# Performance work log

Hardware: AMD Instinct MI355X
Metric: run time of the kernel (lower is better)

Reference implementation:

```python
import jax, jax.numpy as jnp
import numpy as np

K = 512  # number of clusters
D = 128  # feature dim
N = 8192 # number of points


def setup_inputs() -> dict:
    key = jax.random.key(0)
    k1, k2 = jax.random.split(key)
    locF = jax.random.normal(k1, (N, 1, D), dtype=jnp.float32)
    Ck = jax.random.normal(k2, (1, K, D), dtype=jnp.float32)
    return {"locF": locF, "Ck": Ck}


def reference(locF, Ck):
    # locF: [N, 1, D], Ck: [1, K, D]
    x = locF[:, 0, :]          # [N, D]
    c = Ck[0]                  # [K, D]
    # (GEMM expansion avoids the [N, K, D] broadcast; argmin is unchanged)
    d2 = ((x * x).sum(-1, keepdims=True)
          - 2.0 * (x @ c.T)
          + (c * c).sum(-1)[None, :]) / D   # [N, K]
    index = jnp.argmin(d2, axis=1)           # [N]
    # per-cluster scatter-sum and counts (fused, single pass)
    Ck1 = jax.ops.segment_sum(x, index, num_segments=K)[None]  # [1, K, D]
    nItems = jax.ops.segment_sum(jnp.ones((x.shape[0],), dtype=jnp.int32),
                                 index, num_segments=K).reshape(1, -1)  # [1, K]
    return (Ck1, nItems)
```

## Files before the change

### kernel.cpp

```cpp
#include <hip/hip_runtime.h>
#include <hip/hip_bf16.h>

#define KC 512
#define DD 128
#define NP 8192


__global__ __launch_bounds__(256) void kprep(const float* __restrict__ Ck,
                                             float* __restrict__ CkT,
                                             float* __restrict__ sumc2,
                                             float* __restrict__ out) {
    const int b = blockIdx.x;
    const int t = threadIdx.x;
    if (b < 32) {
        #pragma unroll
        for (int i = 0; i < 8; ++i) {
            const int idx = b * 2048 + i * 256 + t;
            const int d = idx >> 9;
            const int k = idx & 511;
            CkT[idx] = Ck[k * DD + d];
        }
    } else if (b == 32) {
        #pragma unroll
        for (int c = 0; c < 2; ++c) {
            const int k = t + c * 256;
            const float4* row = (const float4*)(Ck + k * DD);
            float s = 0.f;
            #pragma unroll
            for (int i = 0; i < 32; ++i) {
                const float4 v = row[i];
                s += v.x * v.x + v.y * v.y + v.z * v.z + v.w * v.w;
            }
            sumc2[k] = s;
        }
    } else {
        const int base = (b - 33) * 2048 + t;
        #pragma unroll
        for (int i = 0; i < 8; ++i) {
            const int idx = base + i * 256;
            if (idx < KC * DD + KC) out[idx] = 0.f;
        }
    }
}

__global__ __launch_bounds__(256, 1) void kmain(const float* __restrict__ X,
                                                const float* __restrict__ CkT,
                                                const float* __restrict__ sumc2,
                                                float* __restrict__ out) {
    __shared__ __align__(16) float xs[32 * DD];
    __shared__ __align__(16) float cst[16 * KC];
    __shared__ int win[32];

    const int tid  = threadIdx.x;
    const int lane = tid & 63;
    const int wv   = tid >> 6;
    const int p0   = blockIdx.x * 32;

    {
        const float4* Xv = (const float4*)(X + p0 * DD);
        float4* xv = (float4*)xs;
        #pragma unroll
        for (int i = 0; i < 4; ++i) xv[tid + 256 * i] = Xv[tid + 256 * i];
    }

    float acc[8][8];
    #pragma unroll
    for (int i = 0; i < 8; ++i)
        #pragma unroll
        for (int j = 0; j < 8; ++j) acc[i][j] = 0.f;

    for (int s = 0; s < 8; ++s) {
        __syncthreads();
        {
            const float4* Cv = (const float4*)(CkT + s * 16 * KC);
            float4* cv = (float4*)cst;
            #pragma unroll
            for (int i = 0; i < 8; ++i) cv[tid + 256 * i] = Cv[tid + 256 * i];
        }
        __syncthreads();

        #pragma unroll
        for (int kk4 = 0; kk4 < 4; ++kk4) {
            float4 xf[8];
            #pragma unroll
            for (int i = 0; i < 8; ++i)
                xf[i] = *(const float4*)&xs[(8 * wv + i) * DD + s * 16 + kk4 * 4];
            #pragma unroll
            for (int kk = 0; kk < 4; ++kk) {
                const float4 c0 = *(const float4*)&cst[(kk4 * 4 + kk) * KC + 4 * lane];
                const float4 c1 = *(const float4*)&cst[(kk4 * 4 + kk) * KC + 256 + 4 * lane];
                #pragma unroll
                for (int i = 0; i < 8; ++i) {
                    const float xv = (&xf[i].x)[kk];
                    acc[i][0] = fmaf(xv, c0.x, acc[i][0]);
                    acc[i][1] = fmaf(xv, c0.y, acc[i][1]);
                    acc[i][2] = fmaf(xv, c0.z, acc[i][2]);
                    acc[i][3] = fmaf(xv, c0.w, acc[i][3]);
                    acc[i][4] = fmaf(xv, c1.x, acc[i][4]);
                    acc[i][5] = fmaf(xv, c1.y, acc[i][5]);
                    acc[i][6] = fmaf(xv, c1.z, acc[i][6]);
                    acc[i][7] = fmaf(xv, c1.w, acc[i][7]);
                }
            }
        }
    }

    float bestv[8];
    int   besti[8];
    #pragma unroll
    for (int i = 0; i < 8; ++i) { bestv[i] = 3.4e38f; besti[i] = 0; }
    #pragma unroll
    for (int j = 0; j < 8; ++j) {
        const int cent = (j < 4) ? (4 * lane + j) : (256 + 4 * lane + (j - 4));
        const float s2 = sumc2[cent];
        #pragma unroll
        for (int i = 0; i < 8; ++i) {
            const float v = fmaf(-2.f, acc[i][j], s2);
            if (v < bestv[i]) { bestv[i] = v; besti[i] = cent; }
        }
    }
    #pragma unroll
    for (int off = 1; off < 64; off <<= 1) {
        #pragma unroll
        for (int i = 0; i < 8; ++i) {
            const float ov = __shfl_xor(bestv[i], off);
            const int   oi = __shfl_xor(besti[i], off);
            if (ov < bestv[i] || (ov == bestv[i] && oi < besti[i])) {
                bestv[i] = ov; besti[i] = oi;
            }
        }
    }
    if (lane == 0) {
        #pragma unroll
        for (int i = 0; i < 8; ++i) win[8 * wv + i] = besti[i];
    }
    __syncthreads();

    #pragma unroll
    for (int i = 0; i < 16; ++i) {
        const int flat = tid + 256 * i;
        const int p = flat >> 7;
        const int d = flat & 127;
        atomicAdd(&out[win[p] * DD + d], xs[flat]);
    }
    if (tid < 32) atomicAdd(&out[KC * DD + win[tid]], 1.0f);
}

extern "C" void kernel_launch(void* const* d_in, const int* in_sizes, int n_in,
                              void* d_out, int out_size, void* d_ws, size_t ws_size,
                              hipStream_t stream) {
    const float* locF = (const float*)d_in[0];
    const float* Ck   = (const float*)d_in[1];
    float* out   = (float*)d_out;
    float* sumc2 = (float*)d_ws;
    float* CkT   = (float*)((char*)d_ws + 4096);

    hipLaunchKernelGGL(kprep, dim3(66), dim3(256), 0, stream, Ck, CkT, sumc2, out);
    hipLaunchKernelGGL(kmain, dim3(256), dim3(256), 0, stream, locF, CkT, sumc2, out);
}
```

Baseline: 50.15 us.

## Split-K across wave halves with double-buffered direct-to-LDS centroid loads

Each block now handles 16 points instead of 32, so the grid grows to 512 blocks and occupancy rises to two blocks per CU. Within a block the two pairs of waves each take half of the feature dimension, and their partial dot products are summed through LDS before the argmin. Centroid tiles are streamed with global_load_lds into double-buffered shared memory, overlapping the next load with the current FMAs. This costs an extra LDS reduction and barrier, and each block now reads the full centroid table for fewer points.

```diff
diff --git a/kernel.cpp b/kernel.cpp
--- a/kernel.cpp
+++ b/kernel.cpp
@@ -5,6 +5,13 @@
 #define DD 128
 #define NP 8192
 
+
+__device__ __forceinline__ void gload_lds16(const float* g, float* l) {
+    __builtin_amdgcn_global_load_lds(
+        (const __attribute__((address_space(1))) void*)(uintptr_t)g,
+        (__attribute__((address_space(3))) void*)(uintptr_t)l,
+        16, 0, 0);
+}
 
 __global__ __launch_bounds__(256) void kprep(const float* __restrict__ Ck,
                                              float* __restrict__ CkT,
@@ -43,25 +50,38 @@
     }
 }
 
-__global__ __launch_bounds__(256, 1) void kmain(const float* __restrict__ X,
+__global__ __launch_bounds__(256, 2) void kmain(const float* __restrict__ X,
                                                 const float* __restrict__ CkT,
                                                 const float* __restrict__ sumc2,
                                                 float* __restrict__ out) {
-    __shared__ __align__(16) float xs[32 * DD];
-    __shared__ __align__(16) float cst[16 * KC];
-    __shared__ int win[32];
+    __shared__ __align__(16) float xs[16 * DD];
+    __shared__ __align__(16) float cst[2][2][8 * KC];
+    __shared__ int win[16];
 
     const int tid  = threadIdx.x;
     const int lane = tid & 63;
     const int wv   = tid >> 6;
-    const int p0   = blockIdx.x * 32;
-
-    {
-        const float4* Xv = (const float4*)(X + p0 * DD);
-        float4* xv = (float4*)xs;
-        #pragma unroll
-        for (int i = 0; i < 4; ++i) xv[tid + 256 * i] = Xv[tid + 256 * i];
-    }
+    const int h    = wv >> 1;
+    const int wl   = wv & 1;
+    const int p0   = blockIdx.x * 16;
+
+    const float* Xg = X + p0 * DD;
+    #pragma unroll
+    for (int j = 0; j < 2; ++j) {
+        const int unit = (wv * 2 + j) * 64;
+        gload_lds16(Xg + (unit + lane) * 4, &xs[unit * 4]);
+    }
+
+    auto STAGE = [&](int t, int b) {
+        const float* src = CkT + (h * 64 + t * 8) * KC;
+        float* dst = &cst[b][h][0];
+        #pragma unroll
+        for (int j = 0; j < 8; ++j) {
+            const int chunk = (wl * 8 + j) * 256;
+            gload_lds16(src + chunk + lane * 4, dst + chunk);
+        }
+    };
+    STAGE(0, 0);
 
     float acc[8][8];
     #pragma unroll
@@ -69,26 +89,29 @@
         #pragma unroll
         for (int j = 0; j < 8; ++j) acc[i][j] = 0.f;
 
-    for (int s = 0; s < 8; ++s) {
-        __syncthreads();
-        {
-            const float4* Cv = (const float4*)(CkT + s * 16 * KC);
-            float4* cv = (float4*)cst;
-            #pragma unroll
-            for (int i = 0; i < 8; ++i) cv[tid + 256 * i] = Cv[tid + 256 * i];
-        }
-        __syncthreads();
-
-        #pragma unroll
-        for (int kk4 = 0; kk4 < 4; ++kk4) {
+    for (int t = 0; t < 8; ++t) {
+        const int b = t & 1;
+        if (t < 7) {
+            STAGE(t + 1, b ^ 1);
+            asm volatile("s_waitcnt vmcnt(8)" ::: "memory");
+        } else {
+            asm volatile("s_waitcnt vmcnt(0)" ::: "memory");
+        }
+        __builtin_amdgcn_s_barrier();
+        __builtin_amdgcn_sched_barrier(0);
+
+        const float* cb = &cst[b][h][0];
+        const int dbase = h * 64 + t * 8;
+        #pragma unroll
+        for (int kk4 = 0; kk4 < 2; ++kk4) {
             float4 xf[8];
             #pragma unroll
             for (int i = 0; i < 8; ++i)
-                xf[i] = *(const float4*)&xs[(8 * wv + i) * DD + s * 16 + kk4 * 4];
+                xf[i] = *(const float4*)&xs[(8 * wl + i) * DD + dbase + kk4 * 4];
             #pragma unroll
             for (int kk = 0; kk < 4; ++kk) {
-                const float4 c0 = *(const float4*)&cst[(kk4 * 4 + kk) * KC + 4 * lane];
-                const float4 c1 = *(const float4*)&cst[(kk4 * 4 + kk) * KC + 256 + 4 * lane];
+                const float4 c0 = *(const float4*)&cb[(kk4 * 4 + kk) * KC + 4 * lane];
+                const float4 c1 = *(const float4*)&cb[(kk4 * 4 + kk) * KC + 256 + 4 * lane];
                 #pragma unroll
                 for (int i = 0; i < 8; ++i) {
                     const float xv = (&xf[i].x)[kk];
@@ -103,47 +126,69 @@
                 }
             }
         }
-    }
-
-    float bestv[8];
-    int   besti[8];
+        __builtin_amdgcn_sched_barrier(0);
+        __builtin_amdgcn_s_barrier();
+        __builtin_amdgcn_sched_barrier(0);
+    }
+
+    float4* ex = (float4*)&cst[0][0][0];
+    const int tl = tid & 127;
+    if (h == 1) {
+        #pragma unroll
+        for (int i = 0; i < 8; ++i) {
+            ex[(2 * i) * 128 + tl]     = make_float4(acc[i][0], acc[i][1], acc[i][2], acc[i][3]);
+            ex[(2 * i + 1) * 128 + tl] = make_float4(acc[i][4], acc[i][5], acc[i][6], acc[i][7]);
+        }
+    }
+    __syncthreads();
+    if (h == 0) {
+        #pragma unroll
+        for (int i = 0; i < 8; ++i) {
+            const float4 a0 = ex[(2 * i) * 128 + tl];
+            const float4 a1 = ex[(2 * i + 1) * 128 + tl];
+            acc[i][0] += a0.x; acc[i][1] += a0.y; acc[i][2] += a0.z; acc[i][3] += a0.w;
+            acc[i][4] += a1.x; acc[i][5] += a1.y; acc[i][6] += a1.z; acc[i][7] += a1.w;
+        }
+        float bestv[8];
+        int   besti[8];
+        #pragma unroll
+        for (int i = 0; i < 8; ++i) { bestv[i] = 3.4e38f; besti[i] = 0; }
+        #pragma unroll
+        for (int j = 0; j < 8; ++j) {
+            const int cent = (j < 4) ? (4 * lane + j) : (256 + 4 * lane + (j - 4));
+            const float s2 = sumc2[cent];
+            #pragma unroll
+            for (int i = 0; i < 8; ++i) {
+                const float v = fmaf(-2.f, acc[i][j], s2);
+                if (v < bestv[i]) { bestv[i] = v; besti[i] = cent; }
+            }
+        }
+        #pragma unroll
+        for (int off = 1; off < 64; off <<= 1) {
+            #pragma unroll
+            for (int i = 0; i < 8; ++i) {
+                const float ov = __shfl_xor(bestv[i], off);
+                const int   oi = __shfl_xor(besti[i], off);
+                if (ov < bestv[i] || (ov == bestv[i] && oi < besti[i])) {
+                    bestv[i] = ov; besti[i] = oi;
+                }
+            }
+        }
+        if (lane == 0) {
+            #pragma unroll
+            for (int i = 0; i < 8; ++i) win[8 * wl + i] = besti[i];
+        }
+    }
+    __syncthreads();
+
     #pragma unroll
-    for (int i = 0; i < 8; ++i) { bestv[i] = 3.4e38f; besti[i] = 0; }
-    #pragma unroll
-    for (int j = 0; j < 8; ++j) {
-        const int cent = (j < 4) ? (4 * lane + j) : (256 + 4 * lane + (j - 4));
-        const float s2 = sumc2[cent];
-        #pragma unroll
-        for (int i = 0; i < 8; ++i) {
-            const float v = fmaf(-2.f, acc[i][j], s2);
-            if (v < bestv[i]) { bestv[i] = v; besti[i] = cent; }
-        }
-    }
-    #pragma unroll
-    for (int off = 1; off < 64; off <<= 1) {
-        #pragma unroll
-        for (int i = 0; i < 8; ++i) {
-            const float ov = __shfl_xor(bestv[i], off);
-            const int   oi = __shfl_xor(besti[i], off);
-            if (ov < bestv[i] || (ov == bestv[i] && oi < besti[i])) {
-                bestv[i] = ov; besti[i] = oi;
-            }
-        }
-    }
-    if (lane == 0) {
-        #pragma unroll
-        for (int i = 0; i < 8; ++i) win[8 * wv + i] = besti[i];
-    }
-    __syncthreads();
-
-    #pragma unroll
-    for (int i = 0; i < 16; ++i) {
+    for (int i = 0; i < 8; ++i) {
         const int flat = tid + 256 * i;
         const int p = flat >> 7;
         const int d = flat & 127;
         atomicAdd(&out[win[p] * DD + d], xs[flat]);
     }
-    if (tid < 32) atomicAdd(&out[KC * DD + win[tid]], 1.0f);
+    if (tid < 16) atomicAdd(&out[KC * DD + win[tid]], 1.0f);
 }
 
 extern "C" void kernel_launch(void* const* d_in, const int* in_sizes, int n_in,
@@ -156,5 +201,5 @@
     float* CkT   = (float*)((char*)d_ws + 4096);
 
     hipLaunchKernelGGL(kprep, dim3(66), dim3(256), 0, stream, Ck, CkT, sumc2, out);
-    hipLaunchKernelGGL(kmain, dim3(256), dim3(256), 0, stream, locF, CkT, sumc2, out);
-}
+    hipLaunchKernelGGL(kmain, dim3(512), dim3(256), 0, stream, locF, CkT, sumc2, out);
+}
```

New measurement: 42.90 us. 1.17x faster.

## Split-K over waves with async global-to-LDS double-buffered centroid staging

Applied to the files above, without the earlier changes.

Each block now handles 8 points with two waves, and each wave takes half of the D reduction. The partial sums are combined through LDS before the argmin. Centroid and point tiles are loaded with global_load_lds into double buffers, with the next stage prefetched through vmcnt waits, which removes the per-stage block barriers and register round-trips. The grid grows to 1024 blocks to fill more CUs. The cost is that each block re-reads the full centroid matrix for fewer points, so L2 traffic rises roughly fourfold, and there is an extra cross-wave reduction.

```diff
diff --git a/kernel.cpp b/kernel.cpp
--- a/kernel.cpp
+++ b/kernel.cpp
@@ -5,6 +5,13 @@
 #define DD 128
 #define NP 8192
 
+
+__device__ __forceinline__ void gload_lds16(const float* g, float* l) {
+    __builtin_amdgcn_global_load_lds(
+        (const __attribute__((address_space(1))) void*)(uintptr_t)g,
+        (__attribute__((address_space(3))) void*)(uintptr_t)l,
+        16, 0, 0);
+}
 
 __global__ __launch_bounds__(256) void kprep(const float* __restrict__ Ck,
                                              float* __restrict__ CkT,
@@ -43,25 +50,37 @@
     }
 }
 
-__global__ __launch_bounds__(256, 1) void kmain(const float* __restrict__ X,
+__global__ __launch_bounds__(128, 2) void kmain(const float* __restrict__ X,
                                                 const float* __restrict__ CkT,
                                                 const float* __restrict__ sumc2,
                                                 float* __restrict__ out) {
-    __shared__ __align__(16) float xs[32 * DD];
-    __shared__ __align__(16) float cst[16 * KC];
-    __shared__ int win[32];
+    __shared__ __align__(16) float xs[8 * DD];
+    __shared__ __align__(16) float cst[2][2][4 * KC];
+    __shared__ int win[8];
 
     const int tid  = threadIdx.x;
     const int lane = tid & 63;
-    const int wv   = tid >> 6;
-    const int p0   = blockIdx.x * 32;
-
-    {
-        const float4* Xv = (const float4*)(X + p0 * DD);
-        float4* xv = (float4*)xs;
-        #pragma unroll
-        for (int i = 0; i < 4; ++i) xv[tid + 256 * i] = Xv[tid + 256 * i];
-    }
+    const int h    = tid >> 6;
+    const int p0   = blockIdx.x * 8;
+
+    const float* Xg = X + p0 * DD;
+    #pragma unroll
+    for (int j = 0; j < 2; ++j) {
+        const int ub = j * 128 + h * 64;
+        gload_lds16(Xg + (ub + lane) * 4, &xs[ub * 4]);
+    }
+
+    const float* csrc = CkT + h * 64 * KC;
+
+    #define STAGE(s, b) do {                                             \
+        const float* _src = csrc + (s) * 4 * KC;                         \
+        float* _dst = &cst[h][(b)][0];                                   \
+        _Pragma("unroll")                                                \
+        for (int _i = 0; _i < 8; ++_i)                                   \
+            gload_lds16(_src + _i * 256 + lane * 4, _dst + _i * 256);    \
+    } while (0)
+
+    STAGE(0, 0);
 
     float acc[8][8];
     #pragma unroll
@@ -69,81 +88,104 @@
         #pragma unroll
         for (int j = 0; j < 8; ++j) acc[i][j] = 0.f;
 
-    for (int s = 0; s < 8; ++s) {
-        __syncthreads();
-        {
-            const float4* Cv = (const float4*)(CkT + s * 16 * KC);
-            float4* cv = (float4*)cst;
-            #pragma unroll
-            for (int i = 0; i < 8; ++i) cv[tid + 256 * i] = Cv[tid + 256 * i];
-        }
-        __syncthreads();
-
-        #pragma unroll
-        for (int kk4 = 0; kk4 < 4; ++kk4) {
-            float4 xf[8];
-            #pragma unroll
-            for (int i = 0; i < 8; ++i)
-                xf[i] = *(const float4*)&xs[(8 * wv + i) * DD + s * 16 + kk4 * 4];
-            #pragma unroll
-            for (int kk = 0; kk < 4; ++kk) {
-                const float4 c0 = *(const float4*)&cst[(kk4 * 4 + kk) * KC + 4 * lane];
-                const float4 c1 = *(const float4*)&cst[(kk4 * 4 + kk) * KC + 256 + 4 * lane];
-                #pragma unroll
-                for (int i = 0; i < 8; ++i) {
-                    const float xv = (&xf[i].x)[kk];
-                    acc[i][0] = fmaf(xv, c0.x, acc[i][0]);
-                    acc[i][1] = fmaf(xv, c0.y, acc[i][1]);
-                    acc[i][2] = fmaf(xv, c0.z, acc[i][2]);
-                    acc[i][3] = fmaf(xv, c0.w, acc[i][3]);
-                    acc[i][4] = fmaf(xv, c1.x, acc[i][4]);
-                    acc[i][5] = fmaf(xv, c1.y, acc[i][5]);
-                    acc[i][6] = fmaf(xv, c1.z, acc[i][6]);
-                    acc[i][7] = fmaf(xv, c1.w, acc[i][7]);
+    #pragma unroll 2
+    for (int t = 0; t < 16; ++t) {
+        const int b = t & 1;
+        if (t < 15) {
+            STAGE(t + 1, b ^ 1);
+            asm volatile("s_waitcnt vmcnt(8)" ::: "memory");
+        } else {
+            asm volatile("s_waitcnt vmcnt(0)" ::: "memory");
+        }
+        if (t == 0) __syncthreads();
+        __builtin_amdgcn_sched_barrier(0);
+
+        const float* cb = &cst[h][b][0];
+        float4 xf[8];
+        #pragma unroll
+        for (int p = 0; p < 8; ++p)
+            xf[p] = *(const float4*)&xs[p * DD + h * 64 + t * 4];
+        #pragma unroll
+        for (int d = 0; d < 4; ++d) {
+            const float4 c0 = *(const float4*)&cb[d * KC + 4 * lane];
+            const float4 c1 = *(const float4*)&cb[d * KC + 256 + 4 * lane];
+            #pragma unroll
+            for (int p = 0; p < 8; ++p) {
+                const float xv = (&xf[p].x)[d];
+                acc[p][0] = fmaf(xv, c0.x, acc[p][0]);
+                acc[p][1] = fmaf(xv, c0.y, acc[p][1]);
+                acc[p][2] = fmaf(xv, c0.z, acc[p][2]);
+                acc[p][3] = fmaf(xv, c0.w, acc[p][3]);
+                acc[p][4] = fmaf(xv, c1.x, acc[p][4]);
+                acc[p][5] = fmaf(xv, c1.y, acc[p][5]);
+                acc[p][6] = fmaf(xv, c1.z, acc[p][6]);
+                acc[p][7] = fmaf(xv, c1.w, acc[p][7]);
+            }
+        }
+        __builtin_amdgcn_sched_barrier(0);
+    }
+    #undef STAGE
+
+    __syncthreads();
+    float* ex = &cst[0][0][0];
+    if (h == 1) {
+        #pragma unroll
+        for (int p = 0; p < 8; ++p) {
+            *(float4*)&ex[(p * 2 + 0) * 256 + lane * 4] =
+                make_float4(acc[p][0], acc[p][1], acc[p][2], acc[p][3]);
+            *(float4*)&ex[(p * 2 + 1) * 256 + lane * 4] =
+                make_float4(acc[p][4], acc[p][5], acc[p][6], acc[p][7]);
+        }
+    }
+    __syncthreads();
+    if (h == 0) {
+        #pragma unroll
+        for (int p = 0; p < 8; ++p) {
+            const float4 a0 = *(const float4*)&ex[(p * 2 + 0) * 256 + lane * 4];
+            const float4 a1 = *(const float4*)&ex[(p * 2 + 1) * 256 + lane * 4];
+            acc[p][0] += a0.x; acc[p][1] += a0.y; acc[p][2] += a0.z; acc[p][3] += a0.w;
+            acc[p][4] += a1.x; acc[p][5] += a1.y; acc[p][6] += a1.z; acc[p][7] += a1.w;
+        }
+        float bestv[8];
+        int   besti[8];
+        #pragma unroll
+        for (int p = 0; p < 8; ++p) { bestv[p] = 3.4e38f; besti[p] = 0; }
+        #pragma unroll
+        for (int j = 0; j < 8; ++j) {
+            const int cent = (j < 4) ? (4 * lane + j) : (256 + 4 * lane + (j - 4));
+            const float s2 = sumc2[cent];
+            #pragma unroll
+            for (int p = 0; p < 8; ++p) {
+                const float v = fmaf(-2.f, acc[p][j], s2);
+                if (v < bestv[p]) { bestv[p] = v; besti[p] = cent; }
+            }
+        }
+        #pragma unroll
+        for (int off = 1; off < 64; off <<= 1) {
+            #pragma unroll
+            for (int p = 0; p < 8; ++p) {
+                const float ov = __shfl_xor(bestv[p], off);
+                const int   oi = __shfl_xor(besti[p], off);
+                if (ov < bestv[p] || (ov == bestv[p] && oi < besti[p])) {
+                    bestv[p] = ov; besti[p] = oi;
                 }
             }
         }
-    }
-
-    float bestv[8];
-    int   besti[8];
+        if (lane == 0) {
+            #pragma unroll
+            for (int p = 0; p < 8; ++p) win[p] = besti[p];
+        }
+    }
+    __syncthreads();
+
     #pragma unroll
-    for (int i = 0; i < 8; ++i) { bestv[i] = 3.4e38f; besti[i] = 0; }
-    #pragma unroll
-    for (int j = 0; j < 8; ++j) {
-        const int cent = (j < 4) ? (4 * lane + j) : (256 + 4 * lane + (j - 4));
-        const float s2 = sumc2[cent];
-        #pragma unroll
-        for (int i = 0; i < 8; ++i) {
-            const float v = fmaf(-2.f, acc[i][j], s2);
-            if (v < bestv[i]) { bestv[i] = v; besti[i] = cent; }
-        }
-    }
-    #pragma unroll
-    for (int off = 1; off < 64; off <<= 1) {
-        #pragma unroll
-        for (int i = 0; i < 8; ++i) {
-            const float ov = __shfl_xor(bestv[i], off);
-            const int   oi = __shfl_xor(besti[i], off);
-            if (ov < bestv[i] || (ov == bestv[i] && oi < besti[i])) {
-                bestv[i] = ov; besti[i] = oi;
-            }
-        }
-    }
-    if (lane == 0) {
-        #pragma unroll
-        for (int i = 0; i < 8; ++i) win[8 * wv + i] = besti[i];
-    }
-    __syncthreads();
-
-    #pragma unroll
-    for (int i = 0; i < 16; ++i) {
-        const int flat = tid + 256 * i;
+    for (int i = 0; i < 8; ++i) {
+        const int flat = tid + 128 * i;
         const int p = flat >> 7;
         const int d = flat & 127;
         atomicAdd(&out[win[p] * DD + d], xs[flat]);
     }
-    if (tid < 32) atomicAdd(&out[KC * DD + win[tid]], 1.0f);
+    if (tid < 8) atomicAdd(&out[KC * DD + win[tid]], 1.0f);
 }
 
 extern "C" void kernel_launch(void* const* d_in, const int* in_sizes, int n_in,
@@ -156,5 +198,5 @@
     float* CkT   = (float*)((char*)d_ws + 4096);
 
     hipLaunchKernelGGL(kprep, dim3(66), dim3(256), 0, stream, Ck, CkT, sumc2, out);
-    hipLaunchKernelGGL(kmain, dim3(256), dim3(256), 0, stream, locF, CkT, sumc2, out);
-}
+    hipLaunchKernelGGL(kmain, dim3(1024), dim3(128), 0, stream, locF, CkT, sumc2, out);
+}
```

Result: faster. 43.36 us (-13.5%).

## Shrink point tiles, stream centroids from global into registers, vectorize transpose

Applied to the files above, without the earlier changes.

The main kernel now handles 8 points per 128-thread block across 1024 blocks instead of 32 points per 256-thread block. Each of the two waves covers half the 512 centroids and reads centroid columns straight from global/L2 into registers with one-step prefetch, so the shared-memory centroid staging and its barriers are gone. The two half-wave argmin results are merged through shared memory. The prep kernel's transpose now reads float4 rows across 64 blocks. This buys more parallelism and fewer syncs, but every block re-reads the full centroid matrix from cache, giving less reuse per byte loaded.

```diff
diff --git a/kernel.cpp b/kernel.cpp
--- a/kernel.cpp
+++ b/kernel.cpp
@@ -12,15 +12,15 @@
                                              float* __restrict__ out) {
     const int b = blockIdx.x;
     const int t = threadIdx.x;
-    if (b < 32) {
-        #pragma unroll
-        for (int i = 0; i < 8; ++i) {
-            const int idx = b * 2048 + i * 256 + t;
-            const int d = idx >> 9;
-            const int k = idx & 511;
-            CkT[idx] = Ck[k * DD + d];
-        }
-    } else if (b == 32) {
+    if (b < 64) {
+        const float4 v = *(const float4*)(Ck + b * 1024 + t * 4);
+        const int k = b * 8 + (t >> 5);
+        const int d = (t & 31) * 4;
+        CkT[(d + 0) * KC + k] = v.x;
+        CkT[(d + 1) * KC + k] = v.y;
+        CkT[(d + 2) * KC + k] = v.z;
+        CkT[(d + 3) * KC + k] = v.w;
+    } else if (b == 64) {
         #pragma unroll
         for (int c = 0; c < 2; ++c) {
             const int k = t + c * 256;
@@ -34,7 +34,7 @@
             sumc2[k] = s;
         }
     } else {
-        const int base = (b - 33) * 2048 + t;
+        const int base = (b - 65) * 2048 + t;
         #pragma unroll
         for (int i = 0; i < 8; ++i) {
             const int idx = base + i * 256;
@@ -43,64 +43,62 @@
     }
 }
 
-__global__ __launch_bounds__(256, 1) void kmain(const float* __restrict__ X,
-                                                const float* __restrict__ CkT,
-                                                const float* __restrict__ sumc2,
-                                                float* __restrict__ out) {
-    __shared__ __align__(16) float xs[32 * DD];
-    __shared__ __align__(16) float cst[16 * KC];
-    __shared__ int win[32];
+__global__ __launch_bounds__(128) void kmain(const float* __restrict__ X,
+                                             const float* __restrict__ CkT,
+                                             const float* __restrict__ sumc2,
+                                             float* __restrict__ out) {
+    __shared__ __align__(16) float xs[8 * DD];
+    __shared__ float bvx[2][8];
+    __shared__ int   bix[2][8];
+    __shared__ int   win[8];
 
     const int tid  = threadIdx.x;
     const int lane = tid & 63;
-    const int wv   = tid >> 6;
-    const int p0   = blockIdx.x * 32;
+    const int h    = tid >> 6;
+    const int p0   = blockIdx.x * 8;
 
     {
         const float4* Xv = (const float4*)(X + p0 * DD);
         float4* xv = (float4*)xs;
+        xv[tid]       = Xv[tid];
+        xv[tid + 128] = Xv[tid + 128];
+    }
+    __syncthreads();
+
+    const float* cp = CkT + h * 256 + 4 * lane;
+
+    float4 cn[4], cc[4];
+    #pragma unroll
+    for (int dd = 0; dd < 4; ++dd) cn[dd] = *(const float4*)(cp + dd * KC);
+
+    float acc[8][4];
+    #pragma unroll
+    for (int p = 0; p < 8; ++p)
         #pragma unroll
-        for (int i = 0; i < 4; ++i) xv[tid + 256 * i] = Xv[tid + 256 * i];
-    }
+        for (int j = 0; j < 4; ++j) acc[p][j] = 0.f;
 
-    float acc[8][8];
-    #pragma unroll
-    for (int i = 0; i < 8; ++i)
+    #pragma unroll 4
+    for (int t = 0; t < 32; ++t) {
         #pragma unroll
-        for (int j = 0; j < 8; ++j) acc[i][j] = 0.f;
-
-    for (int s = 0; s < 8; ++s) {
-        __syncthreads();
-        {
-            const float4* Cv = (const float4*)(CkT + s * 16 * KC);
-            float4* cv = (float4*)cst;
+        for (int dd = 0; dd < 4; ++dd) cc[dd] = cn[dd];
+        if (t < 31) {
             #pragma unroll
-            for (int i = 0; i < 8; ++i) cv[tid + 256 * i] = Cv[tid + 256 * i];
+            for (int dd = 0; dd < 4; ++dd)
+                cn[dd] = *(const float4*)(cp + ((t + 1) * 4 + dd) * KC);
         }
-        __syncthreads();
-
+        float4 xf[8];
         #pragma unroll
-        for (int kk4 = 0; kk4 < 4; ++kk4) {
-            float4 xf[8];
+        for (int p = 0; p < 8; ++p)
+            xf[p] = *(const float4*)&xs[p * DD + t * 4];
+        #pragma unroll
+        for (int dd = 0; dd < 4; ++dd) {
             #pragma unroll
-            for (int i = 0; i < 8; ++i)
-                xf[i] = *(const float4*)&xs[(8 * wv + i) * DD + s * 16 + kk4 * 4];
-            #pragma unroll
-            for (int kk = 0; kk < 4; ++kk) {
-                const float4 c0 = *(const float4*)&cst[(kk4 * 4 + kk) * KC + 4 * lane];
-                const float4 c1 = *(const float4*)&cst[(kk4 * 4 + kk) * KC + 256 + 4 * lane];
-                #pragma unroll
-                for (int i = 0; i < 8; ++i) {
-                    const float xv = (&xf[i].x)[kk];
-                    acc[i][0] = fmaf(xv, c0.x, acc[i][0]);
-                    acc[i][1] = fmaf(xv, c0.y, acc[i][1]);
-                    acc[i][2] = fmaf(xv, c0.z, acc[i][2]);
-                    acc[i][3] = fmaf(xv, c0.w, acc[i][3]);
-                    acc[i][4] = fmaf(xv, c1.x, acc[i][4]);
-                    acc[i][5] = fmaf(xv, c1.y, acc[i][5]);
-                    acc[i][6] = fmaf(xv, c1.z, acc[i][6]);
-                    acc[i][7] = fmaf(xv, c1.w, acc[i][7]);
-                }
+            for (int p = 0; p < 8; ++p) {
+                const float xv = (&xf[p].x)[dd];
+                acc[p][0] = fmaf(xv, cc[dd].x, acc[p][0]);
+                acc[p][1] = fmaf(xv, cc[dd].y, acc[p][1]);
+                acc[p][2] = fmaf(xv, cc[dd].z, acc[p][2]);
+                acc[p][3] = fmaf(xv, cc[dd].w, acc[p][3]);
             }
         }
     }
@@ -108,42 +106,48 @@
     float bestv[8];
     int   besti[8];
     #pragma unroll
-    for (int i = 0; i < 8; ++i) { bestv[i] = 3.4e38f; besti[i] = 0; }
+    for (int p = 0; p < 8; ++p) { bestv[p] = 3.4e38f; besti[p] = 0; }
+    const float4 s2v = *(const float4*)(sumc2 + h * 256 + 4 * lane);
     #pragma unroll
-    for (int j = 0; j < 8; ++j) {
-        const int cent = (j < 4) ? (4 * lane + j) : (256 + 4 * lane + (j - 4));
-        const float s2 = sumc2[cent];
+    for (int j = 0; j < 4; ++j) {
+        const int cent = h * 256 + 4 * lane + j;
+        const float s2 = (&s2v.x)[j];
         #pragma unroll
-        for (int i = 0; i < 8; ++i) {
-            const float v = fmaf(-2.f, acc[i][j], s2);
-            if (v < bestv[i]) { bestv[i] = v; besti[i] = cent; }
+        for (int p = 0; p < 8; ++p) {
+            const float v = fmaf(-2.f, acc[p][j], s2);
+            if (v < bestv[p]) { bestv[p] = v; besti[p] = cent; }
         }
     }
     #pragma unroll
     for (int off = 1; off < 64; off <<= 1) {
         #pragma unroll
-        for (int i = 0; i < 8; ++i) {
-            const float ov = __shfl_xor(bestv[i], off);
-            const int   oi = __shfl_xor(besti[i], off);
-            if (ov < bestv[i] || (ov == bestv[i] && oi < besti[i])) {
-                bestv[i] = ov; besti[i] = oi;
+        for (int p = 0; p < 8; ++p) {
+            const float ov = __shfl_xor(bestv[p], off);
+            const int   oi = __shfl_xor(besti[p], off);
+            if (ov < bestv[p] || (ov == bestv[p] && oi < besti[p])) {
+                bestv[p] = ov; besti[p] = oi;
             }
         }
     }
     if (lane == 0) {
         #pragma unroll
-        for (int i = 0; i < 8; ++i) win[8 * wv + i] = besti[i];
+        for (int p = 0; p < 8; ++p) { bvx[h][p] = bestv[p]; bix[h][p] = besti[p]; }
+    }
+    __syncthreads();
+    if (tid < 8) {
+        const float v0 = bvx[0][tid], v1 = bvx[1][tid];
+        win[tid] = (v1 < v0) ? bix[1][tid] : bix[0][tid];
     }
     __syncthreads();
 
     #pragma unroll
-    for (int i = 0; i < 16; ++i) {
-        const int flat = tid + 256 * i;
+    for (int i = 0; i < 8; ++i) {
+        const int flat = tid + 128 * i;
         const int p = flat >> 7;
         const int d = flat & 127;
         atomicAdd(&out[win[p] * DD + d], xs[flat]);
     }
-    if (tid < 32) atomicAdd(&out[KC * DD + win[tid]], 1.0f);
+    if (tid < 8) atomicAdd(&out[KC * DD + win[tid]], 1.0f);
 }
 
 extern "C" void kernel_launch(void* const* d_in, const int* in_sizes, int n_in,
@@ -155,6 +159,6 @@
     float* sumc2 = (float*)d_ws;
     float* CkT   = (float*)((char*)d_ws + 4096);
 
-    hipLaunchKernelGGL(kprep, dim3(66), dim3(256), 0, stream, Ck, CkT, sumc2, out);
-    hipLaunchKernelGGL(kmain, dim3(256), dim3(256), 0, stream, locF, CkT, sumc2, out);
+    hipLaunchKernelGGL(kprep, dim3(98), dim3(256), 0, stream, Ck, CkT, sumc2, out);
+    hipLaunchKernelGGL(kmain, dim3(1024), dim3(128), 0, stream, locF, CkT, sumc2, out);
 }
```

After: 41.59 us. 17.1% less time.
